# Performance work log

Hardware: AMD Instinct MI355X
Metric: run time of the kernel (lower is better)

Reference implementation:

```python
import jax, jax.numpy as jnp
import numpy as np


def setup_inputs() -> dict:
    key = jax.random.key(0)
    k1, k2, k3, k4, k5 = jax.random.split(key, 5)
    B, d, T = 32, 512, 2048
    return {
        "G": jax.random.normal(k1, (B, 4 * d, T), dtype=jnp.float32),
        "m1_tensor": jax.random.normal(k2, (B, d, T), dtype=jnp.float32),
        "m2_tensor": jax.random.normal(k3, (B, d, T), dtype=jnp.float32),
        "wp1": jax.random.normal(k4, (1, 5 * d), dtype=jnp.float32),
        "wp2": jax.random.normal(k5, (1, 5 * d), dtype=jnp.float32),
    }


def reference(G, m1_tensor, m2_tensor, wp1, wp2):
    # Original: per-example concat([G, m], axis=0) -> [5d, T], then per-position
    # dot(wp, column) loop -> [T]. Equivalent single contraction over feature dim.
    GM1 = jnp.concatenate([G, m1_tensor], axis=1)  # [B, 5d, T]
    GM2 = jnp.concatenate([G, m2_tensor], axis=1)  # [B, 5d, T]
    p1 = jnp.einsum("f,bft->bt", wp1[0], GM1)      # [B, T]
    p2 = jnp.einsum("f,bft->bt", wp2[0], GM2)      # [B, T]
    p1_pred = jax.nn.softmax(p1, axis=-1)
    p2_pred = jax.nn.softmax(p2, axis=-1)
    return jnp.stack([p1_pred, p2_pred], axis=1)   # [B, 2, T]
```

## Files before the change

kernel.cpp:

```cpp
#include <hip/hip_runtime.h>

#define BB     32
#define DD     512
#define FOURD  2048
#define FIVED  2560
#define TT     2048
#define TV     (TT / 4)
#define FSPLIT 10
#define ROWS   256

__global__ __launch_bounds__(256, 4) void partial_kernel(
    const float* __restrict__ G,
    const float* __restrict__ m1,
    const float* __restrict__ m2,
    const float* __restrict__ wp1,
    const float* __restrict__ wp2,
    float* __restrict__ ws)
{
    __shared__ float s_w1[ROWS];
    __shared__ float s_w2[ROWS];
    __shared__ float4 red1[4][64];
    __shared__ float4 red2[4][64];

    const int tid   = threadIdx.x;
    const int tc    = blockIdx.x;
    const int ys    = blockIdx.y;
    const int b     = blockIdx.z;
    const int fbase = ys * ROWS;

    if (tid < ROWS) {
        s_w1[tid] = wp1[fbase + tid];
        s_w2[tid] = wp2[fbase + tid];
    }
    __syncthreads();

    const int tg = tid & 63;
    const int fp = tid >> 6;
    const int tv = tc * 64 + tg;

    float4 acc1 = make_float4(0.f, 0.f, 0.f, 0.f);
    float4 acc2 = make_float4(0.f, 0.f, 0.f, 0.f);

    if (ys < 8) {
        const float4* Gv = (const float4*)(G + (size_t)b * FOURD * TT);
        const int r0 = fbase + fp * 64;
        #pragma unroll 8
        for (int i = 0; i < 64; ++i) {
            const float4 g = Gv[(size_t)(r0 + i) * TV + tv];
            const float w1 = s_w1[fp * 64 + i];
            const float w2 = s_w2[fp * 64 + i];
            acc1.x += w1 * g.x; acc1.y += w1 * g.y; acc1.z += w1 * g.z; acc1.w += w1 * g.w;
            acc2.x += w2 * g.x; acc2.y += w2 * g.y; acc2.z += w2 * g.z; acc2.w += w2 * g.w;
        }
    } else {
        const float4* m1v = (const float4*)(m1 + (size_t)b * DD * TT);
        const float4* m2v = (const float4*)(m2 + (size_t)b * DD * TT);
        const int r0 = (fbase - FOURD) + fp * 64;
        #pragma unroll 4
        for (int i = 0; i < 64; ++i) {
            const float4 a = m1v[(size_t)(r0 + i) * TV + tv];
            const float4 c = m2v[(size_t)(r0 + i) * TV + tv];
            const float w1 = s_w1[fp * 64 + i];
            const float w2 = s_w2[fp * 64 + i];
            acc1.x += w1 * a.x; acc1.y += w1 * a.y; acc1.z += w1 * a.z; acc1.w += w1 * a.w;
            acc2.x += w2 * c.x; acc2.y += w2 * c.y; acc2.z += w2 * c.z; acc2.w += w2 * c.w;
        }
    }

    red1[fp][tg] = acc1;
    red2[fp][tg] = acc2;
    __syncthreads();

    if (tid < 128) {
        const int which = tid >> 6;
        const int g     = tid & 63;
        float4 s = make_float4(0.f, 0.f, 0.f, 0.f);
        #pragma unroll
        for (int p = 0; p < 4; ++p) {
            const float4 v = which ? red2[p][g] : red1[p][g];
            s.x += v.x; s.y += v.y; s.z += v.z; s.w += v.w;
        }
        float4* o = (float4*)ws
                  + ((size_t)b * 2 * FSPLIT + (size_t)which * FSPLIT + ys) * TV
                  + tc * 64 + g;
        *o = s;
    }
}

__global__ __launch_bounds__(256) void reduce_softmax_kernel(
    const float* __restrict__ ws, float* __restrict__ out)
{
    const int b     = blockIdx.x >> 1;
    const int which = blockIdx.x & 1;
    const int tid   = threadIdx.x;
    const float* base = ws + ((size_t)b * 2 * FSPLIT + (size_t)which * FSPLIT) * TT;

    float v[8];
    float mx = -INFINITY;
    #pragma unroll
    for (int i = 0; i < 8; ++i) {
        const int t = tid + i * 256;
        float s = 0.f;
        #pragma unroll
        for (int p = 0; p < FSPLIT; ++p) s += base[(size_t)p * TT + t];
        v[i] = s;
        mx = fmaxf(mx, s);
    }

    #pragma unroll
    for (int off = 32; off > 0; off >>= 1)
        mx = fmaxf(mx, __shfl_xor(mx, off, 64));

    __shared__ float sred[4];
    const int wave = tid >> 6;
    if ((tid & 63) == 0) sred[wave] = mx;
    __syncthreads();
    if (tid == 0)
        sred[0] = fmaxf(fmaxf(sred[0], sred[1]), fmaxf(sred[2], sred[3]));
    __syncthreads();
    mx = sred[0];
    __syncthreads();

    float sum = 0.f;
    #pragma unroll
    for (int i = 0; i < 8; ++i) {
        v[i] = __expf(v[i] - mx);
        sum += v[i];
    }
    #pragma unroll
    for (int off = 32; off > 0; off >>= 1)
        sum += __shfl_xor(sum, off, 64);
    if ((tid & 63) == 0) sred[wave] = sum;
    __syncthreads();
    if (tid == 0)
        sred[0] = sred[0] + sred[1] + sred[2] + sred[3];
    __syncthreads();
    const float inv = 1.0f / sred[0];

    float* p = out + ((size_t)b * 2 + which) * TT;
    #pragma unroll
    for (int i = 0; i < 8; ++i)
        p[tid + i * 256] = v[i] * inv;
}

extern "C" void kernel_launch(void* const* d_in, const int* in_sizes, int n_in,
                              void* d_out, int out_size, void* d_ws, size_t ws_size,
                              hipStream_t stream) {
    const float* G   = (const float*)d_in[0];
    const float* m1  = (const float*)d_in[1];
    const float* m2  = (const float*)d_in[2];
    const float* wp1 = (const float*)d_in[3];
    const float* wp2 = (const float*)d_in[4];
    float* out = (float*)d_out;
    float* ws  = (float*)d_ws;

    dim3 grid1(TT / 256, FSPLIT, BB);
    partial_kernel<<<grid1, 256, 0, stream>>>(G, m1, m2, wp1, wp2, ws);
    reduce_softmax_kernel<<<BB * 2, 256, 0, stream>>>(ws, out);
}
```

Measured before the change: 835.1 us.

## Fuse reduction and softmax into partial kernel via last-block atomic counter

Merges the separate reduce/softmax kernel into the main partial-dot kernel. Each block bumps a per-batch atomic counter after a threadfence, and the last block for a batch sums the split partials and computes both softmaxes with float4 loads and stores. Pointer arithmetic in the inner loops is also hoisted into base pointers. This removes one kernel launch and its tail, but adds a memset launch and an atomic/fence per block.

```diff
diff --git a/kernel.cpp b/kernel.cpp
--- a/kernel.cpp
+++ b/kernel.cpp
@@ -3,24 +3,30 @@
 #define BB     32
 #define DD     512
 #define FOURD  2048
-#define FIVED  2560
 #define TT     2048
-#define TV     (TT / 4)
+#define TVROW  (TT / 4)
 #define FSPLIT 10
 #define ROWS   256
+#define NBLK_PER_B (8 * FSPLIT)
+#define PART_BYTES ((size_t)BB * 2 * FSPLIT * TT * 4)
 
-__global__ __launch_bounds__(256, 4) void partial_kernel(
+__global__ __launch_bounds__(256, 4) void fused_kernel(
     const float* __restrict__ G,
     const float* __restrict__ m1,
     const float* __restrict__ m2,
     const float* __restrict__ wp1,
     const float* __restrict__ wp2,
-    float* __restrict__ ws)
+    float* __restrict__ ws,
+    unsigned int* __restrict__ counters,
+    float* __restrict__ out)
 {
     __shared__ float s_w1[ROWS];
     __shared__ float s_w2[ROWS];
     __shared__ float4 red1[4][64];
     __shared__ float4 red2[4][64];
+    __shared__ int s_last;
+    __shared__ float s_red[4];
+    __shared__ float s_red2[4];
 
     const int tid   = threadIdx.x;
     const int tc    = blockIdx.x;
@@ -42,24 +48,24 @@
     float4 acc2 = make_float4(0.f, 0.f, 0.f, 0.f);
 
     if (ys < 8) {
-        const float4* Gv = (const float4*)(G + (size_t)b * FOURD * TT);
-        const int r0 = fbase + fp * 64;
+        const float4* Gp = (const float4*)(G + (size_t)b * FOURD * TT)
+                         + (size_t)(fbase + fp * 64) * TVROW + tv;
         #pragma unroll 8
         for (int i = 0; i < 64; ++i) {
-            const float4 g = Gv[(size_t)(r0 + i) * TV + tv];
+            const float4 g = Gp[(size_t)i * TVROW];
             const float w1 = s_w1[fp * 64 + i];
             const float w2 = s_w2[fp * 64 + i];
             acc1.x += w1 * g.x; acc1.y += w1 * g.y; acc1.z += w1 * g.z; acc1.w += w1 * g.w;
             acc2.x += w2 * g.x; acc2.y += w2 * g.y; acc2.z += w2 * g.z; acc2.w += w2 * g.w;
         }
     } else {
-        const float4* m1v = (const float4*)(m1 + (size_t)b * DD * TT);
-        const float4* m2v = (const float4*)(m2 + (size_t)b * DD * TT);
         const int r0 = (fbase - FOURD) + fp * 64;
+        const float4* m1p = (const float4*)(m1 + (size_t)b * DD * TT) + (size_t)r0 * TVROW + tv;
+        const float4* m2p = (const float4*)(m2 + (size_t)b * DD * TT) + (size_t)r0 * TVROW + tv;
         #pragma unroll 4
         for (int i = 0; i < 64; ++i) {
-            const float4 a = m1v[(size_t)(r0 + i) * TV + tv];
-            const float4 c = m2v[(size_t)(r0 + i) * TV + tv];
+            const float4 a = m1p[(size_t)i * TVROW];
+            const float4 c = m2p[(size_t)i * TVROW];
             const float w1 = s_w1[fp * 64 + i];
             const float w2 = s_w2[fp * 64 + i];
             acc1.x += w1 * a.x; acc1.y += w1 * a.y; acc1.z += w1 * a.z; acc1.w += w1 * a.w;
@@ -81,66 +87,70 @@
             s.x += v.x; s.y += v.y; s.z += v.z; s.w += v.w;
         }
         float4* o = (float4*)ws
-                  + ((size_t)b * 2 * FSPLIT + (size_t)which * FSPLIT + ys) * TV
+                  + ((size_t)b * 2 * FSPLIT + (size_t)which * FSPLIT + ys) * TVROW
                   + tc * 64 + g;
         *o = s;
     }
-}
 
-__global__ __launch_bounds__(256) void reduce_softmax_kernel(
-    const float* __restrict__ ws, float* __restrict__ out)
-{
-    const int b     = blockIdx.x >> 1;
-    const int which = blockIdx.x & 1;
-    const int tid   = threadIdx.x;
-    const float* base = ws + ((size_t)b * 2 * FSPLIT + (size_t)which * FSPLIT) * TT;
+    __threadfence();
+    __syncthreads();
+    if (tid == 0) {
+        const unsigned int old = atomicAdd(&counters[b], 1u);
+        s_last = (old == NBLK_PER_B - 1);
+    }
+    __syncthreads();
+    if (!s_last) return;
+    __threadfence();
 
-    float v[8];
+    const int which = tid >> 7;
+    const int t2    = tid & 127;
+    const float4* basev = (const float4*)ws + ((size_t)b * 2 + which) * FSPLIT * TVROW;
+
+    float4 v4[4];
     float mx = -INFINITY;
     #pragma unroll
-    for (int i = 0; i < 8; ++i) {
-        const int t = tid + i * 256;
-        float s = 0.f;
+    for (int j = 0; j < 4; ++j) {
+        const int idx = t2 + j * 128;
+        float4 s = make_float4(0.f, 0.f, 0.f, 0.f);
         #pragma unroll
-        for (int p = 0; p < FSPLIT; ++p) s += base[(size_t)p * TT + t];
-        v[i] = s;
-        mx = fmaxf(mx, s);
+        for (int p = 0; p < FSPLIT; ++p) {
+            const float4 t = basev[(size_t)p * TVROW + idx];
+            s.x += t.x; s.y += t.y; s.z += t.z; s.w += t.w;
+        }
+        v4[j] = s;
+        mx = fmaxf(mx, fmaxf(fmaxf(s.x, s.y), fmaxf(s.z, s.w)));
     }
 
     #pragma unroll
     for (int off = 32; off > 0; off >>= 1)
         mx = fmaxf(mx, __shfl_xor(mx, off, 64));
-
-    __shared__ float sred[4];
-    const int wave = tid >> 6;
-    if ((tid & 63) == 0) sred[wave] = mx;
+    if ((tid & 63) == 0) s_red[tid >> 6] = mx;
     __syncthreads();
-    if (tid == 0)
-        sred[0] = fmaxf(fmaxf(sred[0], sred[1]), fmaxf(sred[2], sred[3]));
-    __syncthreads();
-    mx = sred[0];
-    __syncthreads();
+    mx = fmaxf(s_red[which * 2], s_red[which * 2 + 1]);
 
     float sum = 0.f;
     #pragma unroll
-    for (int i = 0; i < 8; ++i) {
-        v[i] = __expf(v[i] - mx);
-        sum += v[i];
+    for (int j = 0; j < 4; ++j) {
+        v4[j].x = __expf(v4[j].x - mx);
+        v4[j].y = __expf(v4[j].y - mx);
+        v4[j].z = __expf(v4[j].z - mx);
+        v4[j].w = __expf(v4[j].w - mx);
+        sum += v4[j].x + v4[j].y + v4[j].z + v4[j].w;
     }
     #pragma unroll
     for (int off = 32; off > 0; off >>= 1)
         sum += __shfl_xor(sum, off, 64);
-    if ((tid & 63) == 0) sred[wave] = sum;
+    if ((tid & 63) == 0) s_red2[tid >> 6] = sum;
     __syncthreads();
-    if (tid == 0)
-        sred[0] = sred[0] + sred[1] + sred[2] + sred[3];
-    __syncthreads();
-    const float inv = 1.0f / sred[0];
+    const float inv = 1.0f / (s_red2[which * 2] + s_red2[which * 2 + 1]);
 
-    float* p = out + ((size_t)b * 2 + which) * TT;
+    float4* op = (float4*)(out + ((size_t)b * 2 + which) * TT);
     #pragma unroll
-    for (int i = 0; i < 8; ++i)
-        p[tid + i * 256] = v[i] * inv;
+    for (int j = 0; j < 4; ++j) {
+        float4 r = v4[j];
+        r.x *= inv; r.y *= inv; r.z *= inv; r.w *= inv;
+        op[t2 + j * 128] = r;
+    }
 }
 
 extern "C" void kernel_launch(void* const* d_in, const int* in_sizes, int n_in,
@@ -153,8 +163,10 @@
     const float* wp2 = (const float*)d_in[4];
     float* out = (float*)d_out;
     float* ws  = (float*)d_ws;
+    unsigned int* counters = (unsigned int*)((char*)d_ws + PART_BYTES);
 
-    dim3 grid1(TT / 256, FSPLIT, BB);
-    partial_kernel<<<grid1, 256, 0, stream>>>(G, m1, m2, wp1, wp2, ws);
-    reduce_softmax_kernel<<<BB * 2, 256, 0, stream>>>(ws, out);
+    hipMemsetAsync(counters, 0, BB * sizeof(unsigned int), stream);
+
+    dim3 grid(TT / 256, FSPLIT, BB);
+    fused_kernel<<<grid, 256, 0, stream>>>(G, m1, m2, wp1, wp2, ws, counters, out);
 }
```

Result: slower. 1.347 ms (+61.3%).
